# Kernel tuning notes

Measured on AMD Instinct MI355X. Metric: run time of the kernel, lower is better.

Reference implementation:

```python
import jax, jax.numpy as jnp
import numpy as np

B, N, D, H = 128, 256, 256, 4  # batch, atoms, feature dim (= fingerprint = input = output), heads
NEG_BIG = -1e10


def setup_inputs() -> dict:
    key = jax.random.key(0)
    ks = jax.random.split(key, 8)
    atom_neighbor_SNN = jax.random.normal(ks[0], (B, N, D), dtype=jnp.float32)
    # 0/1 adjacency (float): mask trick exp(x*-1e10)*-1e10 expects binary entries
    x_full_atom_neighbors = jax.random.randint(ks[1], (B, N, N), 0, 2).astype(jnp.float32)
    # shared neighbor_fc: Linear(D, D)
    lim = 1.0 / np.sqrt(D)
    fc_w = jax.random.uniform(ks[2], (D, D), jnp.float32, -lim, lim)
    fc_b = jnp.zeros((D,), jnp.float32)
    # per-head kernels (xavier_uniform)
    xav = np.sqrt(6.0 / (D + D))
    kernels = jax.random.uniform(ks[3], (H, D, D), jnp.float32, -xav, xav)
    # attention kernels (2D, 1) split into self/neigh halves, xavier on (2D,1)
    xav_a = np.sqrt(6.0 / (2 * D + 1))
    att_self = jax.random.uniform(ks[4], (H, D), jnp.float32, -xav_a, xav_a)
    att_neigh = jax.random.uniform(ks[5], (H, D), jnp.float32, -xav_a, xav_a)
    epsilons = jnp.full((H,), 0.6, jnp.float32)
    biases = jnp.zeros((H, D), jnp.float32)
    att_biases = jnp.zeros((H,), jnp.float32)
    return {
        "atom_neighbor_SNN": atom_neighbor_SNN,
        "x_full_atom_neighbors": x_full_atom_neighbors,
        "fc_w": fc_w, "fc_b": fc_b,
        "kernels": kernels,
        "att_self": att_self, "att_neigh": att_neigh,
        "epsilons": epsilons, "biases": biases, "att_biases": att_biases,
    }


def reference(atom_neighbor_SNN, x_full_atom_neighbors, fc_w, fc_b, kernels,
              att_self, att_neigh, epsilons, biases, att_biases):
    x = x_full_atom_neighbors                      # [B,N,N]
    atom = atom_neighbor_SNN                       # [B,N,D]
    diag = jnp.diagonal(x, axis1=-2, axis2=-1)     # [B,N]
    # new_x[h] = x + eye*diag*(eps[h]-1); so new_x[h] @ atom = x@atom + (eps[h]-1)*diag[:,:,None]*atom
    base = jnp.einsum('bnm,bmd->bnd', x, atom)     # [B,N,D]
    diagterm = diag[..., None] * atom              # [B,N,D]
    nf = base[None] + (epsilons - 1.0)[:, None, None, None] * diagterm[None]  # [H,B,N,D]
    h = jax.nn.leaky_relu(jnp.einsum('hbnd,df->hbnf', nf, fc_w) + fc_b, 0.01)  # shared fc, leaky_relu
    feat = jnp.einsum('hbnf,hfo->hbno', h, kernels) + biases[:, None, None, :]  # [H,B,N,D]
    a_s = jnp.einsum('hbno,ho->hbn', feat, att_self) + att_biases[:, None, None]
    a_n = jnp.einsum('hbno,ho->hbn', feat, att_neigh)
    att = jax.nn.elu(a_s[..., :, None] + a_n[..., None, :])  # [H,B,N,N]
    mask = jnp.exp(x * NEG_BIG) * NEG_BIG                     # 0 on edges, -1e10 off edges
    att = jax.nn.softmax(att + mask[None], axis=-1)
    # dropout: identity (eval mode)
    node = jnp.einsum('hbij,hbjo->hbio', att, feat)           # [H,B,N,D]
    out = jnp.moveaxis(node, 0, 2).reshape(node.shape[1], node.shape[2], H * node.shape[3])  # concat heads -> [B,N,H*D]
    return out, att[-1]
```

## Files before the change

### kernel.cpp

```cpp
#include <hip/hip_runtime.h>

typedef __attribute__((ext_vector_type(8))) short bf16x8;
typedef __attribute__((ext_vector_type(4))) short short4v;
typedef __attribute__((ext_vector_type(4))) float f32x4;


__device__ __forceinline__ float b2f(short s){
  unsigned u = ((unsigned)(unsigned short)s) << 16;
  return __builtin_bit_cast(float, u);
}
__device__ __forceinline__ short f2b(float f){
  unsigned u = __builtin_bit_cast(unsigned, f);
  u = (u + 0x7FFFu + ((u >> 16) & 1u)) >> 16;
  return (short)(unsigned short)u;
}

#define SWZ(row, bytecol) ((((row) * 512) + (bytecol)) ^ (((row) & 7) << 4))

__global__ __launch_bounds__(256) void ktrans(const float* __restrict__ fcw, const float* __restrict__ kers,
                                              short* __restrict__ WT, short* __restrict__ KhT){
  __shared__ float tile[32][33];
  int z = blockIdx.z;
  const float* src = (z == 0) ? fcw : (kers + (z-1)*65536);
  short* dst = (z == 0) ? WT : (KhT + (z-1)*65536);
  int x0 = blockIdx.x*32, y0 = blockIdx.y*32;
  int tx = threadIdx.x & 31, ty = threadIdx.x >> 5;
  #pragma unroll
  for (int i = 0; i < 32; i += 8) tile[ty+i][tx] = src[(y0+ty+i)*256 + x0+tx];
  __syncthreads();
  #pragma unroll
  for (int i = 0; i < 32; i += 8) dst[(x0+ty+i)*256 + y0+tx] = f2b(tile[tx][ty+i]);
}

__global__ __launch_bounds__(256) void kprep(const float* __restrict__ atom, const float* __restrict__ x,
                                             short* __restrict__ atom_bf, short* __restrict__ xbf,
                                             unsigned* __restrict__ xbits, float* __restrict__ diag){
  int b = blockIdx.y;
  int row = blockIdx.x*32 + (threadIdx.x >> 3);
  int seg = threadIdx.x & 7;
  if (blockIdx.z == 0){
    const float* p = atom + b*65536 + row*256 + seg*32;
    short* q = atom_bf + b*65536 + row*256 + seg*32;
    #pragma unroll
    for (int k = 0; k < 4; k++){
      f32x4 a = ((const f32x4*)p)[k*2], c = ((const f32x4*)p)[k*2+1];
      bf16x8 o;
      #pragma unroll
      for (int e = 0; e < 4; e++){ o[e] = f2b(a[e]); o[4+e] = f2b(c[e]); }
      ((bf16x8*)q)[k] = o;
    }
  } else {
    const float* p = x + b*65536 + row*256 + seg*32;
    float v[32];
    #pragma unroll
    for (int k = 0; k < 8; k++){
      f32x4 qv = ((const f32x4*)p)[k];
      #pragma unroll
      for (int e = 0; e < 4; e++) v[k*4+e] = qv[e];
    }
    unsigned bits = 0u;
    #pragma unroll
    for (int e = 0; e < 32; e++) if (v[e] > 0.5f) bits |= (1u << e);
    xbits[(b*256 + row)*8 + seg] = bits;
    short* q = xbf + b*65536 + row*256 + seg*32;
    #pragma unroll
    for (int k = 0; k < 4; k++){
      bf16x8 o;
      #pragma unroll
      for (int e = 0; e < 8; e++) o[e] = f2b(v[k*8+e]);
      ((bf16x8*)q)[k] = o;
    }
    if ((row >> 5) == seg) diag[b*256 + row] = v[row & 31];
  }
}

__global__ __launch_bounds__(256) void kG2(const short* __restrict__ WT, const short* __restrict__ atomb,
                                           short* __restrict__ G2T, short* __restrict__ G2nf){
  int b = blockIdx.y;
  int tr = (blockIdx.x >> 1) * 128, tc = (blockIdx.x & 1) * 128;
  int lane = threadIdx.x & 63, wave = threadIdx.x >> 6;
  int wr = (wave >> 1) * 64, wc = (wave & 1) * 64;
  const short* Y = atomb + b * 65536;
  int r0 = tr + wr + (lane & 15);
  int c0 = tc + wc + (lane & 15);
  int koff = (lane >> 4) * 8;
  f32x4 acc[4][4] = {};
  for (int k0 = 0; k0 < 256; k0 += 32){
    bf16x8 af[4], bfr[4];
    #pragma unroll
    for (int i = 0; i < 4; i++) af[i]  = *(const bf16x8*)(WT + (r0 + i*16)*256 + k0 + koff);
    #pragma unroll
    for (int j = 0; j < 4; j++) bfr[j] = *(const bf16x8*)(Y  + (c0 + j*16)*256 + k0 + koff);
    #pragma unroll
    for (int i = 0; i < 4; i++)
      #pragma unroll
      for (int j = 0; j < 4; j++)
        acc[i][j] = __builtin_amdgcn_mfma_f32_16x16x32_bf16(af[i], bfr[j], acc[i][j], 0, 0, 0);
  }
  int fi0 = tr + wr + (lane >> 4) * 4;
  int mj0 = tc + wc + (lane & 15);
  #pragma unroll
  for (int i = 0; i < 4; i++)
    #pragma unroll
    for (int j = 0; j < 4; j++){
      short4v v;
      #pragma unroll
      for (int r = 0; r < 4; r++) v[r] = f2b(acc[i][j][r]);
      *(short4v*)(G2nf + b*65536 + (mj0 + j*16)*256 + fi0 + i*16) = v;
      #pragma unroll
      for (int r = 0; r < 4; r++)
        G2T[b*65536 + (fi0 + i*16 + r)*256 + mj0 + j*16] = v[r];
    }
}

__global__ __launch_bounds__(256) void kG1(const short* __restrict__ G2T, const short* __restrict__ xbf,
                                           short* __restrict__ G1){
  int b = blockIdx.y;
  int tr = (blockIdx.x >> 1) * 128, tc = (blockIdx.x & 1) * 128;
  int lane = threadIdx.x & 63, wave = threadIdx.x >> 6;
  int wr = (wave >> 1) * 64, wc = (wave & 1) * 64;
  const short* X = G2T + b * 65536;
  const short* Y = xbf + b * 65536;
  int r0 = tr + wr + (lane & 15);
  int c0 = tc + wc + (lane & 15);
  int koff = (lane >> 4) * 8;
  f32x4 acc[4][4] = {};
  for (int k0 = 0; k0 < 256; k0 += 32){
    bf16x8 af[4], bfr[4];
    #pragma unroll
    for (int i = 0; i < 4; i++) af[i]  = *(const bf16x8*)(X + (r0 + i*16)*256 + k0 + koff);
    #pragma unroll
    for (int j = 0; j < 4; j++) bfr[j] = *(const bf16x8*)(Y + (c0 + j*16)*256 + k0 + koff);
    #pragma unroll
    for (int i = 0; i < 4; i++)
      #pragma unroll
      for (int j = 0; j < 4; j++)
        acc[i][j] = __builtin_amdgcn_mfma_f32_16x16x32_bf16(af[i], bfr[j], acc[i][j], 0, 0, 0);
  }
  int fi0 = tr + wr + (lane >> 4) * 4;
  int nj0 = tc + wc + (lane & 15);
  #pragma unroll
  for (int i = 0; i < 4; i++)
    #pragma unroll
    for (int j = 0; j < 4; j++){
      short4v v;
      #pragma unroll
      for (int r = 0; r < 4; r++) v[r] = f2b(acc[i][j][r]);
      *(short4v*)(G1 + b*65536 + (nj0 + j*16)*256 + fi0 + i*16) = v;
    }
}

__global__ __launch_bounds__(512, 1) void kHead(const short* __restrict__ KhT, const short* __restrict__ G1,
                                                const short* __restrict__ G2nf, const float* __restrict__ diag,
                                                const float* __restrict__ fcb, const float* __restrict__ epsv,
                                                const float* __restrict__ biases, const float* __restrict__ atts,
                                                const float* __restrict__ attn, const float* __restrict__ attbv,
                                                const unsigned* __restrict__ xbits,
                                                float* __restrict__ out, float* __restrict__ out2){
  __shared__ __align__(16) char featS[131072];
  __shared__ __align__(16) char scratch[20480];
  __shared__ float asvL[256], anvL[256], fcbL[256];

  short (*h1s)[40] = (short(*)[40])scratch;
  char* Pb0 = scratch;
  char* Pb1 = scratch + 8192;
  float (*red_s)[64] = (float(*)[64])(scratch + 16384);
  float (*red_n)[64] = (float(*)[64])(scratch + 16384 + 2048);

  int wg = blockIdx.x;
  int xcd = wg & 7, idx = wg >> 3;
  int b = xcd + ((idx >> 2) << 3);
  int h = idx & 3;
  int tid = threadIdx.x, lane = tid & 63, w = tid >> 6;
  float epsm1 = epsv[h] - 1.0f;
  const short* KA  = KhT + h*65536;
  const short* G1b = G1  + b*65536;
  const short* G2b = G2nf + b*65536;

  {
    int o = tid >> 1, half = (tid & 1) * 128;
    #pragma unroll
    for (int q = 0; q < 16; q++){
      int kk = half + q*8;
      bf16x8 v = *(const bf16x8*)(KA + o*256 + kk);
      *(bf16x8*)(featS + SWZ(o, kk*2)) = v;
    }
    if (tid < 256) fcbL[tid] = fcb[tid];
  }

  int nl = tid >> 1, rkk = (tid & 1) * 16;
  float cj = epsm1 * diag[b*256 + nl];

  int wro = (w >> 2) * 128;
  int wn  = (w & 3) * 64;
  int lr = lane & 15, lq = lane >> 4;
  int koff = lq * 8;

  bf16x8 p1a = *(const bf16x8*)(G1b + nl*256 + rkk);
  bf16x8 p1b = *(const bf16x8*)(G1b + nl*256 + rkk + 8);
  bf16x8 p2a = *(const bf16x8*)(G2b + nl*256 + rkk);
  bf16x8 p2b = *(const bf16x8*)(G2b + nl*256 + rkk + 8);

  f32x4 acc[4][8] = {};
  for (int t = 0; t < 8; t++){
    int k0 = t*32;
    {
      bf16x8 o1, o2;
      #pragma unroll
      for (int e = 0; e < 8; e++){
        float v = b2f(p1a[e]) + cj*b2f(p2a[e]) + fcbL[k0 + rkk + e];
        v = v > 0.f ? v : 0.01f*v;
        o1[e] = f2b(v);
      }
      #pragma unroll
      for (int e = 0; e < 8; e++){
        float v = b2f(p1b[e]) + cj*b2f(p2b[e]) + fcbL[k0 + rkk + 8 + e];
        v = v > 0.f ? v : 0.01f*v;
        o2[e] = f2b(v);
      }
      *(bf16x8*)&h1s[nl][rkk] = o1;
      *(bf16x8*)&h1s[nl][rkk + 8] = o2;
    }
    __syncthreads();
    if (t < 7){
      int kn = k0 + 32;
      p1a = *(const bf16x8*)(G1b + nl*256 + kn + rkk);
      p1b = *(const bf16x8*)(G1b + nl*256 + kn + rkk + 8);
      p2a = *(const bf16x8*)(G2b + nl*256 + kn + rkk);
      p2b = *(const bf16x8*)(G2b + nl*256 + kn + rkk + 8);
    }
    bf16x8 af[4];
    #pragma unroll
    for (int j = 0; j < 4; j++) af[j] = *(const bf16x8*)&h1s[wn + j*16 + lr][koff];
    #pragma unroll
    for (int i = 0; i < 8; i++){
      bf16x8 bfv = *(const bf16x8*)(featS + SWZ(wro + i*16 + lr, (k0 + koff)*2));
      #pragma unroll
      for (int j = 0; j < 4; j++)
        acc[j][i] = __builtin_amdgcn_mfma_f32_16x16x32_bf16(af[j], bfv, acc[j][i], 0, 0, 0);
    }
    __syncthreads();
  }

  float ps[4][4] = {}, pn[4][4] = {};
  #pragma unroll
  for (int i = 0; i < 8; i++){
    int od = wro + i*16 + lr;
    float bi  = biases[h*256 + od];
    float wsv = atts[h*256 + od];
    float wnv = attn[h*256 + od];
    #pragma unroll
    for (int j = 0; j < 4; j++){
      short4v sv;
      #pragma unroll
      for (int r = 0; r < 4; r++){
        float fv = acc[j][i][r] + bi;
        sv[r] = f2b(fv);
        ps[j][r] += fv * wsv;
        pn[j][r] += fv * wnv;
      }
      *(short4v*)(featS + SWZ(od, (wn + j*16 + lq*4)*2) ) = sv;
    }
  }
  #pragma unroll
  for (int j = 0; j < 4; j++)
    #pragma unroll
    for (int r = 0; r < 4; r++){
      float s = ps[j][r], nv = pn[j][r];
      s += __shfl_xor(s, 1); s += __shfl_xor(s, 2); s += __shfl_xor(s, 4); s += __shfl_xor(s, 8);
      nv += __shfl_xor(nv, 1); nv += __shfl_xor(nv, 2); nv += __shfl_xor(nv, 4); nv += __shfl_xor(nv, 8);
      ps[j][r] = s; pn[j][r] = nv;
    }
  __syncthreads();
  if (lr == 0){
    #pragma unroll
    for (int j = 0; j < 4; j++)
      #pragma unroll
      for (int r = 0; r < 4; r++){
        red_s[w][j*16 + lq*4 + r] = ps[j][r];
        red_n[w][j*16 + lq*4 + r] = pn[j][r];
      }
  }
  __syncthreads();
  if (tid < 256){
    int q = tid >> 6, nn = tid & 63;
    asvL[tid] = red_s[q][nn] + red_s[q+4][nn] + attbv[h];
    anvL[tid] = red_n[q][nn] + red_n[q+4][nn];
  }
  __syncthreads();

  int row = tid >> 5, seg = tid & 31;
  #pragma unroll 1
  for (int pre = 0; pre < 1; pre++){
    int i = row;
    float as_i = asvL[i];
    unsigned bits = xbits[(b*256 + i)*8 + (seg >> 2)];
    int sh = (seg & 3) * 8;
    float Lv[8]; float mx = -3.0e38f;
    #pragma unroll
    for (int e = 0; e < 8; e++){
      float s = as_i + anvL[seg*8 + e];
      float el = s > 0.f ? s : (__expf(s) - 1.0f);
      float L = el + (((bits >> (sh + e)) & 1u) ? 0.f : -1.0e10f);
      Lv[e] = L; mx = fmaxf(mx, L);
    }
    mx = fmaxf(mx, __shfl_xor(mx, 1)); mx = fmaxf(mx, __shfl_xor(mx, 2));
    mx = fmaxf(mx, __shfl_xor(mx, 4)); mx = fmaxf(mx, __shfl_xor(mx, 8));
    mx = fmaxf(mx, __shfl_xor(mx, 16));
    float sum = 0.f;
    #pragma unroll
    for (int e = 0; e < 8; e++){ float p = __expf(Lv[e] - mx); Lv[e] = p; sum += p; }
    sum += __shfl_xor(sum, 1); sum += __shfl_xor(sum, 2); sum += __shfl_xor(sum, 4);
    sum += __shfl_xor(sum, 8); sum += __shfl_xor(sum, 16);
    float inv = 1.0f / sum;
    bf16x8 pv;
    #pragma unroll
    for (int e = 0; e < 8; e++) pv[e] = f2b(Lv[e] * inv);
    *(bf16x8*)(Pb0 + SWZ(row, seg*16)) = pv;
    if (h == 3){
      float* o2 = out2 + b*65536 + i*256 + seg*8;
      f32x4 v0, v1;
      #pragma unroll
      for (int e = 0; e < 4; e++){ v0[e] = Lv[e]*inv; v1[e] = Lv[4+e]*inv; }
      *(f32x4*)(o2) = v0; *(f32x4*)(o2 + 4) = v1;
    }
  }

  int o0w = w * 32;
  for (int t = 0; t < 16; t++){
    __syncthreads();
    int it0 = t * 16;
    char* Pr = (t & 1) ? Pb1 : Pb0;
    f32x4 a2[2] = {};
    for (int k0 = 0; k0 < 256; k0 += 32){
      bf16x8 bfp = *(const bf16x8*)(Pr + SWZ(lr, (k0 + koff)*2));
      #pragma unroll
      for (int ii = 0; ii < 2; ii++){
        bf16x8 afv = *(const bf16x8*)(featS + SWZ(o0w + ii*16 + lr, (k0 + koff)*2));
        a2[ii] = __builtin_amdgcn_mfma_f32_16x16x32_bf16(afv, bfp, a2[ii], 0, 0, 0);
      }
    }
    #pragma unroll
    for (int ii = 0; ii < 2; ii++)
      *(f32x4*)(out + (size_t)(b*256 + it0 + lr)*1024 + h*256 + o0w + ii*16 + lq*4) = a2[ii];

    if (t < 15){
      char* Pw = (t & 1) ? Pb0 : Pb1;
      int i = it0 + 16 + row;
      float as_i = asvL[i];
      unsigned bits = xbits[(b*256 + i)*8 + (seg >> 2)];
      int sh = (seg & 3) * 8;
      float Lv[8]; float mx = -3.0e38f;
      #pragma unroll
      for (int e = 0; e < 8; e++){
        float s = as_i + anvL[seg*8 + e];
        float el = s > 0.f ? s : (__expf(s) - 1.0f);
        float L = el + (((bits >> (sh + e)) & 1u) ? 0.f : -1.0e10f);
        Lv[e] = L; mx = fmaxf(mx, L);
      }
      mx = fmaxf(mx, __shfl_xor(mx, 1)); mx = fmaxf(mx, __shfl_xor(mx, 2));
      mx = fmaxf(mx, __shfl_xor(mx, 4)); mx = fmaxf(mx, __shfl_xor(mx, 8));
      mx = fmaxf(mx, __shfl_xor(mx, 16));
      float sum = 0.f;
      #pragma unroll
      for (int e = 0; e < 8; e++){ float p = __expf(Lv[e] - mx); Lv[e] = p; sum += p; }
      sum += __shfl_xor(sum, 1); sum += __shfl_xor(sum, 2); sum += __shfl_xor(sum, 4);
      sum += __shfl_xor(sum, 8); sum += __shfl_xor(sum, 16);
      float inv = 1.0f / sum;
      bf16x8 pv;
      #pragma unroll
      for (int e = 0; e < 8; e++) pv[e] = f2b(Lv[e] * inv);
      *(bf16x8*)(Pw + SWZ(row, seg*16)) = pv;
      if (h == 3){
        float* o2 = out2 + b*65536 + i*256 + seg*8;
        f32x4 v0, v1;
        #pragma unroll
        for (int e = 0; e < 4; e++){ v0[e] = Lv[e]*inv; v1[e] = Lv[4+e]*inv; }
        *(f32x4*)(o2) = v0; *(f32x4*)(o2 + 4) = v1;
      }
    }
  }
}

extern "C" void kernel_launch(void* const* d_in, const int* in_sizes, int n_in,
                              void* d_out, int out_size, void* d_ws, size_t ws_size,
                              hipStream_t stream) {
  const float* atom   = (const float*)d_in[0];
  const float* x      = (const float*)d_in[1];
  const float* fc_w   = (const float*)d_in[2];
  const float* fc_b   = (const float*)d_in[3];
  const float* kers   = (const float*)d_in[4];
  const float* att_s  = (const float*)d_in[5];
  const float* att_n  = (const float*)d_in[6];
  const float* eps    = (const float*)d_in[7];
  const float* biases = (const float*)d_in[8];
  const float* att_b  = (const float*)d_in[9];

  char* w = (char*)d_ws;
  short* WT      = (short*)(w);
  short* KhT     = (short*)(w + 131072);
  float* diag    = (float*)(w + 655360);
  unsigned* xbits= (unsigned*)(w + 786432);
  short* atomG1  = (short*)(w + 1835008);
  short* xbf     = (short*)(w + 18612224);
  short* G2T     = (short*)(w + 35389440);
  short* G2nf    = (short*)(w + 52166656);

  float* out  = (float*)d_out;
  float* out2 = out + 33554432;

  ktrans<<<dim3(8, 8, 5), 256, 0, stream>>>(fc_w, kers, WT, KhT);
  kprep<<<dim3(8, 128, 2), 256, 0, stream>>>(atom, x, atomG1, xbf, xbits, diag);
  kG2<<<dim3(4, 128), 256, 0, stream>>>(WT, atomG1, G2T, G2nf);
  kG1<<<dim3(4, 128), 256, 0, stream>>>(G2T, xbf, atomG1);

  kHead<<<dim3(512), 512, 0, stream>>>(KhT, atomG1, G2nf, diag, fc_b, eps,
                                       biases, att_s, att_n, att_b, xbits, out, out2);
}
```

Measured before the change: 174.0 us.

## Fuse G2 and G1 GEMMs via LDS and feed head MFMA directly from global

Merges the two per-batch GEMM kernels into one kernel. The G2 tile is kept in swizzled shared memory and consumed directly by the G1 product, so the G2T global round-trip and one launch disappear. In the head kernel, the leaky-relu input fragments are now built per wave straight from global G1/G2 loads instead of a shared h1s staging buffer, which removes two barriers per k-step. Adjacency bits are also cached in LDS for the softmax loop. The trade-off is redundant global loads of G1/G2 across waves and a grid of only 256 blocks at one block per CU for the fused GEMM.

Result: no change. 171.2 us (-1.6%).

```diff
diff --git a/kernel.cpp b/kernel.cpp
--- a/kernel.cpp
+++ b/kernel.cpp
@@ -74,80 +74,77 @@
   }
 }
 
-__global__ __launch_bounds__(256) void kG2(const short* __restrict__ WT, const short* __restrict__ atomb,
-                                           short* __restrict__ G2T, short* __restrict__ G2nf){
-  int b = blockIdx.y;
-  int tr = (blockIdx.x >> 1) * 128, tc = (blockIdx.x & 1) * 128;
-  int lane = threadIdx.x & 63, wave = threadIdx.x >> 6;
-  int wr = (wave >> 1) * 64, wc = (wave & 1) * 64;
-  const short* Y = atomb + b * 65536;
-  int r0 = tr + wr + (lane & 15);
-  int c0 = tc + wc + (lane & 15);
-  int koff = (lane >> 4) * 8;
-  f32x4 acc[4][4] = {};
-  for (int k0 = 0; k0 < 256; k0 += 32){
-    bf16x8 af[4], bfr[4];
-    #pragma unroll
-    for (int i = 0; i < 4; i++) af[i]  = *(const bf16x8*)(WT + (r0 + i*16)*256 + k0 + koff);
-    #pragma unroll
-    for (int j = 0; j < 4; j++) bfr[j] = *(const bf16x8*)(Y  + (c0 + j*16)*256 + k0 + koff);
+__global__ __launch_bounds__(512, 1) void kG12(const short* __restrict__ WT, const short* __restrict__ atomb,
+                                               const short* __restrict__ xbf,
+                                               short* __restrict__ G2nf, short* __restrict__ G1){
+  __shared__ __align__(16) char G2s[65536];
+  int wg = blockIdx.x;
+  int xcd = wg & 7, idx = wg >> 3;
+  int b  = xcd + ((idx >> 1) << 3);
+  int fh = idx & 1;
+  int tid = threadIdx.x, lane = tid & 63, w = tid >> 6;
+  int lr = lane & 15, lq = lane >> 4, koff = lq * 8;
+
+  {
+    int wm = (w >> 1) * 64, wf = (w & 1) * 64;
+    const short* Ab = atomb + b*65536;
+    const short* Bw = WT + (fh*128 + wf)*256;
+    f32x4 acc[4][4] = {};
+    for (int k0 = 0; k0 < 256; k0 += 32){
+      bf16x8 af[4], bfr[4];
+      #pragma unroll
+      for (int i = 0; i < 4; i++) af[i]  = *(const bf16x8*)(Ab + (wm + i*16 + lr)*256 + k0 + koff);
+      #pragma unroll
+      for (int j = 0; j < 4; j++) bfr[j] = *(const bf16x8*)(Bw + (j*16 + lr)*256 + k0 + koff);
+      #pragma unroll
+      for (int i = 0; i < 4; i++)
+        #pragma unroll
+        for (int j = 0; j < 4; j++)
+          acc[i][j] = __builtin_amdgcn_mfma_f32_16x16x32_bf16(af[i], bfr[j], acc[i][j], 0, 0, 0);
+    }
     #pragma unroll
     for (int i = 0; i < 4; i++)
       #pragma unroll
-      for (int j = 0; j < 4; j++)
-        acc[i][j] = __builtin_amdgcn_mfma_f32_16x16x32_bf16(af[i], bfr[j], acc[i][j], 0, 0, 0);
-  }
-  int fi0 = tr + wr + (lane >> 4) * 4;
-  int mj0 = tc + wc + (lane & 15);
-  #pragma unroll
-  for (int i = 0; i < 4; i++)
-    #pragma unroll
-    for (int j = 0; j < 4; j++){
-      short4v v;
-      #pragma unroll
-      for (int r = 0; r < 4; r++) v[r] = f2b(acc[i][j][r]);
-      *(short4v*)(G2nf + b*65536 + (mj0 + j*16)*256 + fi0 + i*16) = v;
-      #pragma unroll
-      for (int r = 0; r < 4; r++)
-        G2T[b*65536 + (fi0 + i*16 + r)*256 + mj0 + j*16] = v[r];
-    }
-}
-
-__global__ __launch_bounds__(256) void kG1(const short* __restrict__ G2T, const short* __restrict__ xbf,
-                                           short* __restrict__ G1){
-  int b = blockIdx.y;
-  int tr = (blockIdx.x >> 1) * 128, tc = (blockIdx.x & 1) * 128;
-  int lane = threadIdx.x & 63, wave = threadIdx.x >> 6;
-  int wr = (wave >> 1) * 64, wc = (wave & 1) * 64;
-  const short* X = G2T + b * 65536;
-  const short* Y = xbf + b * 65536;
-  int r0 = tr + wr + (lane & 15);
-  int c0 = tc + wc + (lane & 15);
-  int koff = (lane >> 4) * 8;
-  f32x4 acc[4][4] = {};
-  for (int k0 = 0; k0 < 256; k0 += 32){
-    bf16x8 af[4], bfr[4];
-    #pragma unroll
-    for (int i = 0; i < 4; i++) af[i]  = *(const bf16x8*)(X + (r0 + i*16)*256 + k0 + koff);
-    #pragma unroll
-    for (int j = 0; j < 4; j++) bfr[j] = *(const bf16x8*)(Y + (c0 + j*16)*256 + k0 + koff);
+      for (int j = 0; j < 4; j++){
+        short4v v;
+        #pragma unroll
+        for (int r = 0; r < 4; r++) v[r] = f2b(acc[i][j][r]);
+        int fl = wf + j*16 + lr;
+        int m0 = wm + i*16 + lq*4;
+        *(short4v*)(G2s + SWZ(fl, m0*2)) = v;
+        #pragma unroll
+        for (int r = 0; r < 4; r++)
+          G2nf[b*65536 + (m0 + r)*256 + fh*128 + fl] = v[r];
+      }
+  }
+  __syncthreads();
+
+  {
+    int wf2 = (w >> 2) * 64, wn2 = (w & 3) * 64;
+    const short* Xb = xbf + b*65536;
+    f32x4 acc[4][4] = {};
+    for (int k0 = 0; k0 < 256; k0 += 32){
+      bf16x8 af[4], bfr[4];
+      #pragma unroll
+      for (int i = 0; i < 4; i++) af[i]  = *(const bf16x8*)(G2s + SWZ(wf2 + i*16 + lr, (k0 + koff)*2));
+      #pragma unroll
+      for (int j = 0; j < 4; j++) bfr[j] = *(const bf16x8*)(Xb + (wn2 + j*16 + lr)*256 + k0 + koff);
+      #pragma unroll
+      for (int i = 0; i < 4; i++)
+        #pragma unroll
+        for (int j = 0; j < 4; j++)
+          acc[i][j] = __builtin_amdgcn_mfma_f32_16x16x32_bf16(af[i], bfr[j], acc[i][j], 0, 0, 0);
+    }
     #pragma unroll
     for (int i = 0; i < 4; i++)
       #pragma unroll
-      for (int j = 0; j < 4; j++)
-        acc[i][j] = __builtin_amdgcn_mfma_f32_16x16x32_bf16(af[i], bfr[j], acc[i][j], 0, 0, 0);
-  }
-  int fi0 = tr + wr + (lane >> 4) * 4;
-  int nj0 = tc + wc + (lane & 15);
-  #pragma unroll
-  for (int i = 0; i < 4; i++)
-    #pragma unroll
-    for (int j = 0; j < 4; j++){
-      short4v v;
-      #pragma unroll
-      for (int r = 0; r < 4; r++) v[r] = f2b(acc[i][j][r]);
-      *(short4v*)(G1 + b*65536 + (nj0 + j*16)*256 + fi0 + i*16) = v;
-    }
+      for (int j = 0; j < 4; j++){
+        short4v v;
+        #pragma unroll
+        for (int r = 0; r < 4; r++) v[r] = f2b(acc[i][j][r]);
+        *(short4v*)(G1 + b*65536 + (wn2 + j*16 + lr)*256 + fh*128 + wf2 + i*16 + lq*4) = v;
+      }
+  }
 }
 
 __global__ __launch_bounds__(512, 1) void kHead(const short* __restrict__ KhT, const short* __restrict__ G1,
@@ -158,14 +155,14 @@
                                                 const unsigned* __restrict__ xbits,
                                                 float* __restrict__ out, float* __restrict__ out2){
   __shared__ __align__(16) char featS[131072];
-  __shared__ __align__(16) char scratch[20480];
+  __shared__ __align__(16) char scratch[24576];
   __shared__ float asvL[256], anvL[256], fcbL[256];
 
-  short (*h1s)[40] = (short(*)[40])scratch;
   char* Pb0 = scratch;
   char* Pb1 = scratch + 8192;
   float (*red_s)[64] = (float(*)[64])(scratch + 16384);
   float (*red_n)[64] = (float(*)[64])(scratch + 16384 + 2048);
+  unsigned* xbitsL = (unsigned*)(scratch + 16384);
 
   int wg = blockIdx.x;
   int xcd = wg & 7, idx = wg >> 3;
@@ -188,50 +185,37 @@
     if (tid < 256) fcbL[tid] = fcb[tid];
   }
 
-  int nl = tid >> 1, rkk = (tid & 1) * 16;
-  float cj = epsm1 * diag[b*256 + nl];
-
   int wro = (w >> 2) * 128;
   int wn  = (w & 3) * 64;
   int lr = lane & 15, lq = lane >> 4;
   int koff = lq * 8;
-
-  bf16x8 p1a = *(const bf16x8*)(G1b + nl*256 + rkk);
-  bf16x8 p1b = *(const bf16x8*)(G1b + nl*256 + rkk + 8);
-  bf16x8 p2a = *(const bf16x8*)(G2b + nl*256 + rkk);
-  bf16x8 p2b = *(const bf16x8*)(G2b + nl*256 + rkk + 8);
+  float cj[4];
+  #pragma unroll
+  for (int j = 0; j < 4; j++) cj[j] = epsm1 * diag[b*256 + wn + j*16 + lr];
+
+  __syncthreads();
 
   f32x4 acc[4][8] = {};
   for (int t = 0; t < 8; t++){
     int k0 = t*32;
-    {
-      bf16x8 o1, o2;
+    f32x4 fb0 = *(const f32x4*)&fcbL[k0 + koff];
+    f32x4 fb1 = *(const f32x4*)&fcbL[k0 + koff + 4];
+    bf16x8 af[4];
+    #pragma unroll
+    for (int j = 0; j < 4; j++){
+      int row = wn + j*16 + lr;
+      bf16x8 g1 = *(const bf16x8*)(G1b + row*256 + k0 + koff);
+      bf16x8 g2 = *(const bf16x8*)(G2b + row*256 + k0 + koff);
+      bf16x8 o;
       #pragma unroll
       for (int e = 0; e < 8; e++){
-        float v = b2f(p1a[e]) + cj*b2f(p2a[e]) + fcbL[k0 + rkk + e];
+        float fbv = (e < 4) ? fb0[e] : fb1[e-4];
+        float v = b2f(g1[e]) + cj[j]*b2f(g2[e]) + fbv;
         v = v > 0.f ? v : 0.01f*v;
-        o1[e] = f2b(v);
-      }
-      #pragma unroll
-      for (int e = 0; e < 8; e++){
-        float v = b2f(p1b[e]) + cj*b2f(p2b[e]) + fcbL[k0 + rkk + 8 + e];
-        v = v > 0.f ? v : 0.01f*v;
-        o2[e] = f2b(v);
-      }
-      *(bf16x8*)&h1s[nl][rkk] = o1;
-      *(bf16x8*)&h1s[nl][rkk + 8] = o2;
-    }
-    __syncthreads();
-    if (t < 7){
-      int kn = k0 + 32;
-      p1a = *(const bf16x8*)(G1b + nl*256 + kn + rkk);
-      p1b = *(const bf16x8*)(G1b + nl*256 + kn + rkk + 8);
-      p2a = *(const bf16x8*)(G2b + nl*256 + kn + rkk);
-      p2b = *(const bf16x8*)(G2b + nl*256 + kn + rkk + 8);
-    }
-    bf16x8 af[4];
-    #pragma unroll
-    for (int j = 0; j < 4; j++) af[j] = *(const bf16x8*)&h1s[wn + j*16 + lr][koff];
+        o[e] = f2b(v);
+      }
+      af[j] = o;
+    }
     #pragma unroll
     for (int i = 0; i < 8; i++){
       bf16x8 bfv = *(const bf16x8*)(featS + SWZ(wro + i*16 + lr, (k0 + koff)*2));
@@ -239,8 +223,8 @@
       for (int j = 0; j < 4; j++)
         acc[j][i] = __builtin_amdgcn_mfma_f32_16x16x32_bf16(af[j], bfv, acc[j][i], 0, 0, 0);
     }
-    __syncthreads();
-  }
+  }
+  __syncthreads();
 
   float ps[4][4] = {}, pn[4][4] = {};
   #pragma unroll
@@ -271,7 +255,6 @@
       nv += __shfl_xor(nv, 1); nv += __shfl_xor(nv, 2); nv += __shfl_xor(nv, 4); nv += __shfl_xor(nv, 8);
       ps[j][r] = s; pn[j][r] = nv;
     }
-  __syncthreads();
   if (lr == 0){
     #pragma unroll
     for (int j = 0; j < 4; j++)
@@ -288,13 +271,18 @@
     anvL[tid] = red_n[q][nn] + red_n[q+4][nn];
   }
   __syncthreads();
+  {
+    const unsigned* xb = xbits + b*2048;
+    #pragma unroll
+    for (int q = 0; q < 4; q++) xbitsL[tid*4 + q] = xb[tid*4 + q];
+  }
+  __syncthreads();
 
   int row = tid >> 5, seg = tid & 31;
-  #pragma unroll 1
-  for (int pre = 0; pre < 1; pre++){
+  {
     int i = row;
     float as_i = asvL[i];
-    unsigned bits = xbits[(b*256 + i)*8 + (seg >> 2)];
+    unsigned bits = xbitsL[i*8 + (seg >> 2)];
     int sh = (seg & 3) * 8;
     float Lv[8]; float mx = -3.0e38f;
     #pragma unroll
@@ -348,7 +336,7 @@
       char* Pw = (t & 1) ? Pb0 : Pb1;
       int i = it0 + 16 + row;
       float as_i = asvL[i];
-      unsigned bits = xbits[(b*256 + i)*8 + (seg >> 2)];
+      unsigned bits = xbitsL[i*8 + (seg >> 2)];
       int sh = (seg & 3) * 8;
       float Lv[8]; float mx = -3.0e38f;
       #pragma unroll
@@ -401,19 +389,17 @@
   short* KhT     = (short*)(w + 131072);
   float* diag    = (float*)(w + 655360);
   unsigned* xbits= (unsigned*)(w + 786432);
-  short* atomG1  = (short*)(w + 1835008);
+  short* atomb   = (short*)(w + 1835008);
   short* xbf     = (short*)(w + 18612224);
-  short* G2T     = (short*)(w + 35389440);
-  short* G2nf    = (short*)(w + 52166656);
+  short* G2nf    = (short*)(w + 35389440);
+  short* G1      = (short*)(w + 52166656);
 
   float* out  = (float*)d_out;
   float* out2 = out + 33554432;
 
   ktrans<<<dim3(8, 8, 5), 256, 0, stream>>>(fc_w, kers, WT, KhT);
-  kprep<<<dim3(8, 128, 2), 256, 0, stream>>>(atom, x, atomG1, xbf, xbits, diag);
-  kG2<<<dim3(4, 128), 256, 0, stream>>>(WT, atomG1, G2T, G2nf);
-  kG1<<<dim3(4, 128), 256, 0, stream>>>(G2T, xbf, atomG1);
-
-  kHead<<<dim3(512), 512, 0, stream>>>(KhT, atomG1, G2nf, diag, fc_b, eps,
+  kprep<<<dim3(8, 128, 2), 256, 0, stream>>>(atom, x, atomb, xbf, xbits, diag);
+  kG12<<<dim3(256), 512, 0, stream>>>(WT, atomb, xbf, G2nf, G1);
+  kHead<<<dim3(512), 512, 0, stream>>>(KhT, G1, G2nf, diag, fc_b, eps,
                                        biases, att_s, att_n, att_b, xbits, out, out2);
 }
```
